# Performance work log

Measured on AMD Instinct MI355X. Metric: run time of the kernel, lower is better.

The kernel has to match this reference:

```python
import jax, jax.numpy as jnp
import numpy as np

N = 50000
E = 800000
D_IN = 128
D_H = 128
D_OUT = 1


def setup_inputs() -> dict:
    key = jax.random.key(0)
    ks = jax.random.split(key, 12)
    x = jax.random.normal(ks[0], (N, D_IN), dtype=jnp.float32)
    edge_index = jax.random.randint(ks[1], (2, E), 0, N, dtype=jnp.int64)
    def glorot(k, shape):
        lim = float(np.sqrt(6.0 / (shape[0] + shape[1])))
        return jax.random.uniform(k, shape, jnp.float32, -lim, lim)
    return {
        "x": x,
        "edge_index": edge_index,
        "W1": glorot(ks[2], (D_IN, D_H)),  "b1": jnp.zeros((D_H,), jnp.float32),
        "W2": glorot(ks[3], (D_H, D_H)),   "b2": jnp.zeros((D_H,), jnp.float32),
        "W3": glorot(ks[4], (D_H, D_H)),   "b3": jnp.zeros((D_H,), jnp.float32),
        "Wfc": glorot(ks[5], (D_H, D_OUT)), "bfc": jnp.zeros((D_OUT,), jnp.float32),
    }


def _gcn_norm(edge_index, num_nodes):
    # Add self-loops (PyG GCNConv default) and compute symmetric normalization
    loops = jnp.arange(num_nodes, dtype=edge_index.dtype)
    src = jnp.concatenate([edge_index[0], loops])
    dst = jnp.concatenate([edge_index[1], loops])
    ones = jnp.ones(src.shape[0], dtype=jnp.float32)
    deg = jax.ops.segment_sum(ones, dst, num_segments=num_nodes)
    dinv = jnp.where(deg > 0, jax.lax.rsqrt(deg), 0.0)
    norm = dinv[src] * dinv[dst]  # [E + N]
    return src, dst, norm


def _gcn_layer(x, W, b, src, dst, norm, num_nodes):
    xw = x @ W                              # [N, out] dense transform first
    msg = xw[src] * norm[:, None]           # gather + scale
    agg = jax.ops.segment_sum(msg, dst, num_segments=num_nodes)  # scatter-add
    return agg + b


def reference(x, edge_index, W1, b1, W2, b2, W3, b3, Wfc, bfc):
    num_nodes = x.shape[0]
    src, dst, norm = _gcn_norm(edge_index, num_nodes)
    h = jax.nn.relu(_gcn_layer(x, W1, b1, src, dst, norm, num_nodes))
    h = jax.nn.relu(_gcn_layer(h, W2, b2, src, dst, norm, num_nodes))
    h = jax.nn.relu(_gcn_layer(h, W3, b3, src, dst, norm, num_nodes))
    return h @ Wfc + bfc  # [N, 1]
```

## Files before the change

kernel.cpp:

```cpp
#include <hip/hip_runtime.h>

#define D 128
#define SCAN_ELEMS 4096

typedef __attribute__((ext_vector_type(8))) short short8;
typedef __attribute__((ext_vector_type(4))) float f32x4;


__global__ void count_kernel(const int* __restrict__ dst, int* __restrict__ deg,
                             int* __restrict__ rank, int e) {
    int i = blockIdx.x * blockDim.x + threadIdx.x;
    if (i < e) rank[i] = atomicAdd(&deg[dst[i]], 1);
}

__global__ __launch_bounds__(256) void scanA_kernel(const int* __restrict__ deg,
                                                    int* __restrict__ blkSums, int n) {
    __shared__ int waveSums[4];
    int t = threadIdx.x;
    int base = blockIdx.x * SCAN_ELEMS + t * 16;
    int s = 0;
    if (base + 16 <= n) {
        const int4* p = reinterpret_cast<const int4*>(deg + base);
        #pragma unroll
        for (int k = 0; k < 4; ++k) {
            int4 v = p[k];
            s += v.x + v.y + v.z + v.w;
        }
    } else {
        for (int k = 0; k < 16; ++k) {
            int i = base + k;
            if (i < n) s += deg[i];
        }
    }
    #pragma unroll
    for (int off = 32; off > 0; off >>= 1) s += __shfl_down(s, off);
    int lane = t & 63, w = t >> 6;
    if (lane == 0) waveSums[w] = s;
    __syncthreads();
    if (t == 0) blkSums[blockIdx.x] = waveSums[0] + waveSums[1] + waveSums[2] + waveSums[3];
}

__global__ __launch_bounds__(256) void scanC_kernel(const int* __restrict__ deg,
                                                    const int* __restrict__ blkSums,
                                                    int* __restrict__ offsets,
                                                    float* __restrict__ dinv, int n, int nblk) {
    __shared__ int waveSums[4];
    __shared__ int blkBase;
    int t = threadIdx.x;
    int lane = t & 63, w = t >> 6;

    if (t < 64) {
        int s = (t < nblk && t < blockIdx.x) ? blkSums[t] : 0;
        #pragma unroll
        for (int off = 32; off > 0; off >>= 1) s += __shfl_down(s, off);
        if (t == 0) blkBase = s;
    }

    int base = blockIdx.x * SCAN_ELEMS + t * 16;
    int v[16];
    int s = 0;
    #pragma unroll
    for (int k = 0; k < 16; ++k) {
        int i = base + k;
        int d = (i < n) ? deg[i] : 0;
        v[k] = d;
        s += d;
    }
    int incl = s;
    #pragma unroll
    for (int off = 1; off < 64; off <<= 1) {
        int u = __shfl_up(incl, off);
        if (lane >= off) incl += u;
    }
    if (lane == 63) waveSums[w] = incl;
    __syncthreads();
    int waveOff = 0;
    for (int i = 0; i < 4; ++i) if (i < w) waveOff += waveSums[i];
    int off0 = blkBase + waveOff + incl - s;

    #pragma unroll
    for (int k = 0; k < 16; ++k) {
        int i = base + k;
        if (i < n) {
            offsets[i] = off0;
            dinv[i] = rsqrtf((float)(v[k] + 1));
            off0 += v[k];
        }
    }
}

__global__ void fill_kernel(const int* __restrict__ src, const int* __restrict__ dst,
                            const int* __restrict__ offsets, const int* __restrict__ rank,
                            int* __restrict__ csr_src, int e) {
    int i = blockIdx.x * blockDim.x + threadIdx.x;
    if (i < e) {
        csr_src[offsets[dst[i]] + rank[i]] = src[i];
    }
}

__device__ inline void f2bf(float f, short& hi, short& lo) {
    union { float f; unsigned u; } a; a.f = f;
    unsigned r = a.u + 0x7fffu + ((a.u >> 16) & 1u);
    hi = (short)(r >> 16);
    union { unsigned u; float f; } h; h.u = ((unsigned)(unsigned short)hi) << 16;
    union { float f; unsigned u; } b; b.f = f - h.f;
    unsigned r2 = b.u + 0x7fffu + ((b.u >> 16) & 1u);
    lo = (short)(r2 >> 16);
}

__device__ inline unsigned enc24(float f) {
    union { float f; unsigned u; } a; a.f = f;
    unsigned r = a.u + 0x7fu + ((a.u >> 8) & 1u);
    return r >> 8;
}

__global__ __launch_bounds__(256) void wsplit_kernel(const float* __restrict__ W1,
                                                     const float* __restrict__ W2,
                                                     const float* __restrict__ W3,
                                                     short* __restrict__ Bsw) {
    int tid = blockIdx.x * 256 + threadIdx.x;
    int layer = tid >> 14;
    int rem = tid & 16383;
    int k = rem >> 7, c = rem & 127;
    const float* Wg = (layer == 0) ? W1 : ((layer == 1) ? W2 : W3);
    float v = Wg[k * 128 + c];
    short hi, lo; f2bf(v, hi, lo);
    int ktile = k >> 5, kk = k & 31, q = kk >> 3, j = kk & 7;
    int ct = c >> 4, mm = c & 15, lane = q * 16 + mm;
    int idx = layer * 32768 + ((ktile * 8 + ct) * 64 + lane) * 8 + j;
    Bsw[idx] = hi;
    Bsw[idx + 16384] = lo;
}

__global__ __launch_bounds__(256) void gemm_kernel(const float* __restrict__ A,
                                                   const short* __restrict__ Bsw,
                                                   const float* __restrict__ dinv,
                                                   unsigned short* __restrict__ xh,
                                                   unsigned char* __restrict__ xl, int n) {
    __shared__ float tile[4][16][132];

    int t = threadIdx.x;
    int w = t >> 6;
    int lane = t & 63;
    int quad = lane >> 4;
    int m = lane & 15;

    int rowBase = blockIdx.x * 64 + w * 16;
    int arow = rowBase + m;
    bool valid = arow < n;
    const float* ap = A + (size_t)(valid ? arow : 0) * D + quad * 8;

    f32x4 acc[8];
    #pragma unroll
    for (int ct = 0; ct < 8; ++ct) acc[ct] = (f32x4){0.f, 0.f, 0.f, 0.f};

    #pragma unroll
    for (int kt = 0; kt < 4; ++kt) {
        short8 a_hi, a_lo;
        {
            float4 f0 = *reinterpret_cast<const float4*>(ap + kt * 32);
            float4 f1 = *reinterpret_cast<const float4*>(ap + kt * 32 + 4);
            float fv[8] = {f0.x, f0.y, f0.z, f0.w, f1.x, f1.y, f1.z, f1.w};
            #pragma unroll
            for (int j = 0; j < 8; ++j) {
                short h, l; f2bf(valid ? fv[j] : 0.f, h, l);
                a_hi[j] = h; a_lo[j] = l;
            }
        }
        const short* bp = Bsw + (kt * 8 * 64 + lane) * 8;
        #pragma unroll
        for (int ct = 0; ct < 8; ++ct) {
            short8 b_hi = *reinterpret_cast<const short8*>(bp + ct * 512);
            short8 b_lo = *reinterpret_cast<const short8*>(bp + 16384 + ct * 512);
            acc[ct] = __builtin_amdgcn_mfma_f32_16x16x32_bf16(a_hi, b_hi, acc[ct], 0, 0, 0);
            acc[ct] = __builtin_amdgcn_mfma_f32_16x16x32_bf16(a_hi, b_lo, acc[ct], 0, 0, 0);
            acc[ct] = __builtin_amdgcn_mfma_f32_16x16x32_bf16(a_lo, b_hi, acc[ct], 0, 0, 0);
        }
    }

    #pragma unroll
    for (int r = 0; r < 4; ++r) {
        int orow = rowBase + quad * 4 + r;
        float s = (orow < n) ? dinv[orow] : 0.f;
        #pragma unroll
        for (int ct = 0; ct < 8; ++ct)
            tile[w][quad * 4 + r][m + ct * 16] = acc[ct][r] * s;
    }
    __syncthreads();

    int r = lane >> 2;
    int c0 = (lane & 3) << 5;
    int gr = rowBase + r;
    if (gr < n) {
        unsigned hu[16], lu[8];
        #pragma unroll
        for (int g = 0; g < 8; ++g) {
            float4 f = *reinterpret_cast<const float4*>(&tile[w][r][c0 + g * 4]);
            unsigned e0 = enc24(f.x), e1 = enc24(f.y), e2 = enc24(f.z), e3 = enc24(f.w);
            hu[g * 2]     = (e0 >> 8) | ((e1 >> 8) << 16);
            hu[g * 2 + 1] = (e2 >> 8) | ((e3 >> 8) << 16);
            lu[g] = (e0 & 0xffu) | ((e1 & 0xffu) << 8) | ((e2 & 0xffu) << 16) | ((e3 & 0xffu) << 24);
        }
        uint4* hp = reinterpret_cast<uint4*>(xh + (size_t)gr * 128 + c0);
        uint4* lp = reinterpret_cast<uint4*>(xl + (size_t)gr * 128 + c0);
        hp[0] = *reinterpret_cast<uint4*>(&hu[0]);
        hp[1] = *reinterpret_cast<uint4*>(&hu[4]);
        hp[2] = *reinterpret_cast<uint4*>(&hu[8]);
        hp[3] = *reinterpret_cast<uint4*>(&hu[12]);
        lp[0] = *reinterpret_cast<uint4*>(&lu[0]);
        lp[1] = *reinterpret_cast<uint4*>(&lu[4]);
    }
}


__device__ inline void g24(const unsigned short* __restrict__ xh,
                           const unsigned char* __restrict__ xl,
                           int row, int c, float4& a) {
    uint2 h2 = *reinterpret_cast<const uint2*>(xh + (size_t)row * 128 + c);
    unsigned lb = *reinterpret_cast<const unsigned*>(xl + (size_t)row * 128 + c);
    union { unsigned u; float f; } v0, v1, v2, v3;
    v0.u = ((h2.x & 0xffffu) << 16) | ((lb & 0xffu) << 8);
    v1.u = (h2.x & 0xffff0000u)     | (((lb >> 8) & 0xffu) << 8);
    v2.u = ((h2.y & 0xffffu) << 16) | (((lb >> 16) & 0xffu) << 8);
    v3.u = (h2.y & 0xffff0000u)     | ((lb >> 24) << 8);
    a.x += v0.f; a.y += v1.f; a.z += v2.f; a.w += v3.f;
}

__global__ __launch_bounds__(256) void agg_kernel(const unsigned short* __restrict__ xh,
                                                  const unsigned char* __restrict__ xl,
                                                  const int* __restrict__ csr_src,
                                                  const int* __restrict__ offsets,
                                                  const int* __restrict__ deg,
                                                  const float* __restrict__ dinv,
                                                  const float* __restrict__ bias,
                                                  float* __restrict__ outp,
                                                  const float* __restrict__ fcw,
                                                  const float* __restrict__ fcb,
                                                  float* __restrict__ fcout,
                                                  int n) {
    int wave = (blockIdx.x * blockDim.x + threadIdx.x) >> 6;
    int lane = threadIdx.x & 63;
    if (wave >= n) return;
    int node = wave;
    int half = lane >> 5;
    int l32  = lane & 31;
    int col  = l32 << 2;

    int base = offsets[node];
    int cnt  = deg[node];

    float di = dinv[node];
    float4 vs = make_float4(0.f, 0.f, 0.f, 0.f);
    g24(xh, xl, node, col, vs);
    float4 b = *reinterpret_cast<const float4*>(bias + col);

    float4 acc0 = make_float4(0.f, 0.f, 0.f, 0.f);
    float4 acc1 = make_float4(0.f, 0.f, 0.f, 0.f);
    float4 acc2 = make_float4(0.f, 0.f, 0.f, 0.f);
    float4 acc3 = make_float4(0.f, 0.f, 0.f, 0.f);

    if (cnt <= 64) {
        int idx = (lane < cnt) ? csr_src[base + lane] : 0;
        int j = 0;
        for (; j + 8 <= cnt; j += 8) {
            int s0 = __shfl(idx, j     + half);
            int s1 = __shfl(idx, j + 2 + half);
            int s2 = __shfl(idx, j + 4 + half);
            int s3 = __shfl(idx, j + 6 + half);
            g24(xh, xl, s0, col, acc0);
            g24(xh, xl, s1, col, acc1);
            g24(xh, xl, s2, col, acc2);
            g24(xh, xl, s3, col, acc3);
        }
        for (; j + 2 <= cnt; j += 2) {
            int s0 = __shfl(idx, j + half);
            g24(xh, xl, s0, col, acc0);
        }
        if (j < cnt) {
            int s0 = __shfl(idx, j);
            if (half == 0) g24(xh, xl, s0, col, acc1);
        }
    } else {
        int j = 0;
        for (; j + 2 <= cnt; j += 2) {
            int s = csr_src[base + j + half];
            g24(xh, xl, s, col, acc0);
        }
        if (j < cnt && half == 0) {
            int s = csr_src[base + j];
            g24(xh, xl, s, col, acc1);
        }
    }

    acc0.x += acc1.x + acc2.x + acc3.x;
    acc0.y += acc1.y + acc2.y + acc3.y;
    acc0.z += acc1.z + acc2.z + acc3.z;
    acc0.w += acc1.w + acc2.w + acc3.w;
    acc0.x += __shfl_down(acc0.x, 32);
    acc0.y += __shfl_down(acc0.y, 32);
    acc0.z += __shfl_down(acc0.z, 32);
    acc0.w += __shfl_down(acc0.w, 32);

    float4 r;
    r.x = fmaxf(di * (acc0.x + vs.x) + b.x, 0.f);
    r.y = fmaxf(di * (acc0.y + vs.y) + b.y, 0.f);
    r.z = fmaxf(di * (acc0.z + vs.z) + b.z, 0.f);
    r.w = fmaxf(di * (acc0.w + vs.w) + b.w, 0.f);

    if (fcw == nullptr) {
        if (half == 0)
            *reinterpret_cast<float4*>(outp + (size_t)node * D + col) = r;
    } else {
        float4 wv = *reinterpret_cast<const float4*>(fcw + col);
        float s = (half == 0) ? (r.x * wv.x + r.y * wv.y + r.z * wv.z + r.w * wv.w) : 0.f;
        #pragma unroll
        for (int off = 32; off > 0; off >>= 1) s += __shfl_down(s, off);
        if (lane == 0) fcout[node] = s + fcb[0];
    }
}


extern "C" void kernel_launch(void* const* d_in, const int* in_sizes, int n_in,
                              void* d_out, int out_size, void* d_ws, size_t ws_size,
                              hipStream_t stream) {
    const float* x   = (const float*)d_in[0];
    const int*   ei  = (const int*)d_in[1];
    const float* W1  = (const float*)d_in[2];
    const float* b1  = (const float*)d_in[3];
    const float* W2  = (const float*)d_in[4];
    const float* b2  = (const float*)d_in[5];
    const float* W3  = (const float*)d_in[6];
    const float* b3  = (const float*)d_in[7];
    const float* Wfc = (const float*)d_in[8];
    const float* bfc = (const float*)d_in[9];
    float* outp = (float*)d_out;

    const int n = in_sizes[0] / D;
    const int e = in_sizes[1] / 2;
    const int* src = ei;
    const int* dst = ei + e;

    char* ws = (char*)d_ws;
    size_t off = 0;
    auto alloc = [&](size_t bytes) {
        void* p = ws + off;
        off += (bytes + 255) & ~(size_t)255;
        return p;
    };
    int*            deg     = (int*)alloc((size_t)n * 4);
    size_t          zero_bytes = off;
    int*            offsets = (int*)alloc((size_t)n * 4);
    float*          dinv    = (float*)alloc((size_t)n * 4);
    int*            blkSums = (int*)alloc(64 * 4);
    short*          Bsw     = (short*)alloc((size_t)3 * 32768 * 2);
    int*            rank    = (int*)alloc((size_t)e * 4);
    int*            csr_src = (int*)alloc((size_t)e * 4);
    unsigned short* xhbuf   = (unsigned short*)alloc((size_t)n * 128 * 2);
    unsigned char*  xlbuf   = (unsigned char*)alloc((size_t)n * 128);
    float*          buf1    = (float*)alloc((size_t)n * D * 4);

    int eb256 = (e + 255) / 256;
    int scan_blocks = (n + SCAN_ELEMS - 1) / SCAN_ELEMS;

    hipMemsetAsync(ws, 0, zero_bytes, stream);
    count_kernel <<<eb256, 256, 0, stream>>>(dst, deg, rank, e);
    scanA_kernel <<<scan_blocks, 256, 0, stream>>>(deg, blkSums, n);
    scanC_kernel <<<scan_blocks, 256, 0, stream>>>(deg, blkSums, offsets, dinv, n, scan_blocks);
    fill_kernel  <<<eb256, 256, 0, stream>>>(src, dst, offsets, rank, csr_src, e);
    wsplit_kernel<<<192, 256, 0, stream>>>(W1, W2, W3, Bsw);

    int gemm_blocks = (n + 63) / 64;
    int agg_blocks  = (n + 3) / 4;

    gemm_kernel<<<gemm_blocks, 256, 0, stream>>>(x, Bsw, dinv, xhbuf, xlbuf, n);
    agg_kernel <<<agg_blocks, 256, 0, stream>>>(xhbuf, xlbuf, csr_src, offsets, deg, dinv, b1, buf1,
                                                nullptr, nullptr, nullptr, n);
    gemm_kernel<<<gemm_blocks, 256, 0, stream>>>(buf1, Bsw + 32768, dinv, xhbuf, xlbuf, n);
    agg_kernel <<<agg_blocks, 256, 0, stream>>>(xhbuf, xlbuf, csr_src, offsets, deg, dinv, b2, buf1,
                                                nullptr, nullptr, nullptr, n);
    gemm_kernel<<<gemm_blocks, 256, 0, stream>>>(buf1, Bsw + 65536, dinv, xhbuf, xlbuf, n);
    agg_kernel <<<agg_blocks, 256, 0, stream>>>(xhbuf, xlbuf, csr_src, offsets, deg, dinv, b3, nullptr,
                                                Wfc, bfc, outp, n);
}
```

Measured before the change: 334.8 us.

## Slice feature layout by column and fuse setup kernels into combined launches

Stores the transformed features in eight column-slice planes (slice-major, 16 columns per row) so the aggregation can run one block per node-group per slice, aiming to keep each slice's gather working set cache-resident. The GEMM now writes the encoded outputs directly with scattered 2-byte and 1-byte stores instead of staging through shared memory. The count and weight-split kernels are merged into one launch, and the CSR fill is merged with the first GEMM, to cut launch count. The final layer keeps a whole-node kernel adapted to the new layout. Risks include uncoalesced narrow stores in the GEMM, re-reading CSR indices eight times, and low lane utilization in small-degree aggregation.

New measurement: 615.9 us. 1.84x slower.

```diff
diff --git a/kernel.cpp b/kernel.cpp
--- a/kernel.cpp
+++ b/kernel.cpp
@@ -6,11 +6,67 @@
 typedef __attribute__((ext_vector_type(8))) short short8;
 typedef __attribute__((ext_vector_type(4))) float f32x4;
 
-
-__global__ void count_kernel(const int* __restrict__ dst, int* __restrict__ deg,
-                             int* __restrict__ rank, int e) {
-    int i = blockIdx.x * blockDim.x + threadIdx.x;
-    if (i < e) rank[i] = atomicAdd(&deg[dst[i]], 1);
+__device__ inline void f2bf(float f, short& hi, short& lo) {
+    union { float f; unsigned u; } a; a.f = f;
+    unsigned r = a.u + 0x7fffu + ((a.u >> 16) & 1u);
+    hi = (short)(r >> 16);
+    union { unsigned u; float f; } h; h.u = ((unsigned)(unsigned short)hi) << 16;
+    union { float f; unsigned u; } b; b.f = f - h.f;
+    unsigned r2 = b.u + 0x7fffu + ((b.u >> 16) & 1u);
+    lo = (short)(r2 >> 16);
+}
+
+__device__ inline unsigned enc24(float f) {
+    union { float f; unsigned u; } a; a.f = f;
+    unsigned r = a.u + 0x7fu + ((a.u >> 8) & 1u);
+    return r >> 8;
+}
+
+__device__ inline void dec4(const unsigned short* __restrict__ xh,
+                            const unsigned char* __restrict__ xl,
+                            unsigned off, float* a) {
+    uint2 h2 = *reinterpret_cast<const uint2*>(xh + off);
+    unsigned lb = *reinterpret_cast<const unsigned*>(xl + off);
+    union { unsigned u; float f; } v0, v1, v2, v3;
+    v0.u = ((h2.x & 0xffffu) << 16) | ((lb & 0xffu) << 8);
+    v1.u = (h2.x & 0xffff0000u)     | (((lb >> 8) & 0xffu) << 8);
+    v2.u = ((h2.y & 0xffffu) << 16) | (((lb >> 16) & 0xffu) << 8);
+    v3.u = (h2.y & 0xffff0000u)     | ((lb >> 24) << 8);
+    a[0] += v0.f; a[1] += v1.f; a[2] += v2.f; a[3] += v3.f;
+}
+
+
+__device__ void wsplit_body(int tid, const float* __restrict__ W1,
+                            const float* __restrict__ W2, const float* __restrict__ W3,
+                            short* __restrict__ Bsw) {
+    int layer = tid >> 14;
+    int rem = tid & 16383;
+    int k = rem >> 7, c = rem & 127;
+    const float* Wg = (layer == 0) ? W1 : ((layer == 1) ? W2 : W3);
+    float v = Wg[k * 128 + c];
+    short hi, lo; f2bf(v, hi, lo);
+    int ktile = k >> 5, kk = k & 31, q = kk >> 3, j = kk & 7;
+    int ct = c >> 4, mm = c & 15, lane = q * 16 + mm;
+    int idx = layer * 32768 + ((ktile * 8 + ct) * 64 + lane) * 8 + j;
+    Bsw[idx] = hi;
+    Bsw[idx + 16384] = lo;
+}
+
+__global__ __launch_bounds__(256) void count_wsplit_kernel(const int* __restrict__ dst,
+                                                           int* __restrict__ deg,
+                                                           int* __restrict__ rank, int e,
+                                                           int nbCount,
+                                                           const float* __restrict__ W1,
+                                                           const float* __restrict__ W2,
+                                                           const float* __restrict__ W3,
+                                                           short* __restrict__ Bsw) {
+    if ((int)blockIdx.x < nbCount) {
+        int i = blockIdx.x * 256 + threadIdx.x;
+        if (i < e) rank[i] = atomicAdd(&deg[dst[i]], 1);
+    } else {
+        int tid = (blockIdx.x - nbCount) * 256 + threadIdx.x;
+        wsplit_body(tid, W1, W2, W3, Bsw);
+    }
 }
 
 __global__ __launch_bounds__(256) void scanA_kernel(const int* __restrict__ deg,
@@ -50,7 +106,7 @@
     int lane = t & 63, w = t >> 6;
 
     if (t < 64) {
-        int s = (t < nblk && t < blockIdx.x) ? blkSums[t] : 0;
+        int s = (t < nblk && t < (int)blockIdx.x) ? blkSums[t] : 0;
         #pragma unroll
         for (int off = 32; off > 0; off >>= 1) s += __shfl_down(s, off);
         if (t == 0) blkBase = s;
@@ -89,63 +145,17 @@
     }
 }
 
-__global__ void fill_kernel(const int* __restrict__ src, const int* __restrict__ dst,
-                            const int* __restrict__ offsets, const int* __restrict__ rank,
-                            int* __restrict__ csr_src, int e) {
-    int i = blockIdx.x * blockDim.x + threadIdx.x;
-    if (i < e) {
-        csr_src[offsets[dst[i]] + rank[i]] = src[i];
-    }
-}
-
-__device__ inline void f2bf(float f, short& hi, short& lo) {
-    union { float f; unsigned u; } a; a.f = f;
-    unsigned r = a.u + 0x7fffu + ((a.u >> 16) & 1u);
-    hi = (short)(r >> 16);
-    union { unsigned u; float f; } h; h.u = ((unsigned)(unsigned short)hi) << 16;
-    union { float f; unsigned u; } b; b.f = f - h.f;
-    unsigned r2 = b.u + 0x7fffu + ((b.u >> 16) & 1u);
-    lo = (short)(r2 >> 16);
-}
-
-__device__ inline unsigned enc24(float f) {
-    union { float f; unsigned u; } a; a.f = f;
-    unsigned r = a.u + 0x7fu + ((a.u >> 8) & 1u);
-    return r >> 8;
-}
-
-__global__ __launch_bounds__(256) void wsplit_kernel(const float* __restrict__ W1,
-                                                     const float* __restrict__ W2,
-                                                     const float* __restrict__ W3,
-                                                     short* __restrict__ Bsw) {
-    int tid = blockIdx.x * 256 + threadIdx.x;
-    int layer = tid >> 14;
-    int rem = tid & 16383;
-    int k = rem >> 7, c = rem & 127;
-    const float* Wg = (layer == 0) ? W1 : ((layer == 1) ? W2 : W3);
-    float v = Wg[k * 128 + c];
-    short hi, lo; f2bf(v, hi, lo);
-    int ktile = k >> 5, kk = k & 31, q = kk >> 3, j = kk & 7;
-    int ct = c >> 4, mm = c & 15, lane = q * 16 + mm;
-    int idx = layer * 32768 + ((ktile * 8 + ct) * 64 + lane) * 8 + j;
-    Bsw[idx] = hi;
-    Bsw[idx + 16384] = lo;
-}
-
-__global__ __launch_bounds__(256) void gemm_kernel(const float* __restrict__ A,
-                                                   const short* __restrict__ Bsw,
-                                                   const float* __restrict__ dinv,
-                                                   unsigned short* __restrict__ xh,
-                                                   unsigned char* __restrict__ xl, int n) {
-    __shared__ float tile[4][16][132];
-
-    int t = threadIdx.x;
+__device__ void gemm_body(int blk, const float* __restrict__ A,
+                          const short* __restrict__ Bsw,
+                          const float* __restrict__ dinv,
+                          unsigned short* __restrict__ xh,
+                          unsigned char* __restrict__ xl, int n, int t) {
     int w = t >> 6;
     int lane = t & 63;
     int quad = lane >> 4;
     int m = lane & 15;
 
-    int rowBase = blockIdx.x * 64 + w * 16;
+    int rowBase = blk * 64 + w * 16;
     int arow = rowBase + m;
     bool valid = arow < n;
     const float* ap = A + (size_t)(valid ? arow : 0) * D + quad * 8;
@@ -167,7 +177,7 @@
                 a_hi[j] = h; a_lo[j] = l;
             }
         }
-        const short* bp = Bsw + (kt * 8 * 64 + lane) * 8;
+        const short* bp = Bsw + (kt * 512 + lane) * 8;
         #pragma unroll
         for (int ct = 0; ct < 8; ++ct) {
             short8 b_hi = *reinterpret_cast<const short8*>(bp + ct * 512);
@@ -180,84 +190,140 @@
 
     #pragma unroll
     for (int r = 0; r < 4; ++r) {
-        int orow = rowBase + quad * 4 + r;
-        float s = (orow < n) ? dinv[orow] : 0.f;
+        int row = rowBase + quad * 4 + r;
+        if (row < n) {
+            float s = dinv[row];
+            #pragma unroll
+            for (int ct = 0; ct < 8; ++ct) {
+                unsigned e24 = enc24(acc[ct][r] * s);
+                unsigned off = ((unsigned)ct * (unsigned)n + (unsigned)row) * 16u + (unsigned)m;
+                xh[off] = (unsigned short)(e24 >> 8);
+                xl[off] = (unsigned char)(e24 & 0xffu);
+            }
+        }
+    }
+}
+
+__global__ __launch_bounds__(256) void gemm_kernel(const float* __restrict__ A,
+                                                   const short* __restrict__ Bsw,
+                                                   const float* __restrict__ dinv,
+                                                   unsigned short* __restrict__ xh,
+                                                   unsigned char* __restrict__ xl, int n) {
+    gemm_body(blockIdx.x, A, Bsw, dinv, xh, xl, n, threadIdx.x);
+}
+
+__global__ __launch_bounds__(256) void fill_gemm_kernel(const int* __restrict__ src,
+                                                        const int* __restrict__ dst,
+                                                        const int* __restrict__ offsets,
+                                                        const int* __restrict__ rank,
+                                                        int* __restrict__ csr_src, int e,
+                                                        int nbFill,
+                                                        const float* __restrict__ A,
+                                                        const short* __restrict__ Bsw,
+                                                        const float* __restrict__ dinv,
+                                                        unsigned short* __restrict__ xh,
+                                                        unsigned char* __restrict__ xl, int n) {
+    if ((int)blockIdx.x < nbFill) {
+        int i = blockIdx.x * 256 + threadIdx.x;
+        if (i < e) csr_src[offsets[dst[i]] + rank[i]] = src[i];
+    } else {
+        gemm_body(blockIdx.x - nbFill, A, Bsw, dinv, xh, xl, n, threadIdx.x);
+    }
+}
+
+__global__ __launch_bounds__(256) void aggs_kernel(const unsigned short* __restrict__ xh,
+                                                   const unsigned char* __restrict__ xl,
+                                                   const int* __restrict__ csr_src,
+                                                   const int* __restrict__ offsets,
+                                                   const int* __restrict__ deg,
+                                                   const float* __restrict__ dinv,
+                                                   const float* __restrict__ bias,
+                                                   float* __restrict__ outp, int n) {
+    int b = blockIdx.x;
+    int slice = b & 7;
+    int w = threadIdx.x >> 6;
+    int node = (b >> 3) * 4 + w;
+    if (node >= n) return;
+    int lane = threadIdx.x & 63;
+    int e16 = lane & 15;
+    int g = lane >> 4;
+
+    unsigned sbase = (unsigned)slice * (unsigned)n;
+    unsigned g4 = (unsigned)(g << 2);
+
+    int base = offsets[node];
+    int cnt  = deg[node];
+    float di = dinv[node];
+
+    float vs[4] = {};
+    dec4(xh, xl, (sbase + (unsigned)node) * 16u + g4, vs);
+    float4 bb = *reinterpret_cast<const float4*>(bias + slice * 16 + (g << 2));
+
+    float a[4] = {};
+    if (cnt <= 64) {
+        int idx = (lane < cnt) ? csr_src[base + lane] : 0;
+        for (int j = 0; j < cnt; j += 16) {
+            int eI = j + e16;
+            int s0 = __shfl(idx, eI);
+            if (eI < cnt)
+                dec4(xh, xl, (sbase + (unsigned)s0) * 16u + g4, a);
+        }
+    } else {
+        for (int j = 0; j < cnt; j += 16) {
+            int eI = j + e16;
+            if (eI < cnt) {
+                int s0 = csr_src[base + eI];
+                dec4(xh, xl, (sbase + (unsigned)s0) * 16u + g4, a);
+            }
+        }
+    }
+
+    #pragma unroll
+    for (int s = 1; s < 16; s <<= 1) {
         #pragma unroll
-        for (int ct = 0; ct < 8; ++ct)
-            tile[w][quad * 4 + r][m + ct * 16] = acc[ct][r] * s;
-    }
-    __syncthreads();
-
-    int r = lane >> 2;
-    int c0 = (lane & 3) << 5;
-    int gr = rowBase + r;
-    if (gr < n) {
-        unsigned hu[16], lu[8];
-        #pragma unroll
-        for (int g = 0; g < 8; ++g) {
-            float4 f = *reinterpret_cast<const float4*>(&tile[w][r][c0 + g * 4]);
-            unsigned e0 = enc24(f.x), e1 = enc24(f.y), e2 = enc24(f.z), e3 = enc24(f.w);
-            hu[g * 2]     = (e0 >> 8) | ((e1 >> 8) << 16);
-            hu[g * 2 + 1] = (e2 >> 8) | ((e3 >> 8) << 16);
-            lu[g] = (e0 & 0xffu) | ((e1 & 0xffu) << 8) | ((e2 & 0xffu) << 16) | ((e3 & 0xffu) << 24);
-        }
-        uint4* hp = reinterpret_cast<uint4*>(xh + (size_t)gr * 128 + c0);
-        uint4* lp = reinterpret_cast<uint4*>(xl + (size_t)gr * 128 + c0);
-        hp[0] = *reinterpret_cast<uint4*>(&hu[0]);
-        hp[1] = *reinterpret_cast<uint4*>(&hu[4]);
-        hp[2] = *reinterpret_cast<uint4*>(&hu[8]);
-        hp[3] = *reinterpret_cast<uint4*>(&hu[12]);
-        lp[0] = *reinterpret_cast<uint4*>(&lu[0]);
-        lp[1] = *reinterpret_cast<uint4*>(&lu[4]);
-    }
-}
-
-
-__device__ inline void g24(const unsigned short* __restrict__ xh,
-                           const unsigned char* __restrict__ xl,
-                           int row, int c, float4& a) {
-    uint2 h2 = *reinterpret_cast<const uint2*>(xh + (size_t)row * 128 + c);
-    unsigned lb = *reinterpret_cast<const unsigned*>(xl + (size_t)row * 128 + c);
-    union { unsigned u; float f; } v0, v1, v2, v3;
-    v0.u = ((h2.x & 0xffffu) << 16) | ((lb & 0xffu) << 8);
-    v1.u = (h2.x & 0xffff0000u)     | (((lb >> 8) & 0xffu) << 8);
-    v2.u = ((h2.y & 0xffffu) << 16) | (((lb >> 16) & 0xffu) << 8);
-    v3.u = (h2.y & 0xffff0000u)     | ((lb >> 24) << 8);
-    a.x += v0.f; a.y += v1.f; a.z += v2.f; a.w += v3.f;
-}
-
-__global__ __launch_bounds__(256) void agg_kernel(const unsigned short* __restrict__ xh,
-                                                  const unsigned char* __restrict__ xl,
-                                                  const int* __restrict__ csr_src,
-                                                  const int* __restrict__ offsets,
-                                                  const int* __restrict__ deg,
-                                                  const float* __restrict__ dinv,
-                                                  const float* __restrict__ bias,
-                                                  float* __restrict__ outp,
-                                                  const float* __restrict__ fcw,
-                                                  const float* __restrict__ fcb,
-                                                  float* __restrict__ fcout,
-                                                  int n) {
+        for (int k = 0; k < 4; ++k) a[k] += __shfl_down(a[k], s);
+    }
+
+    if (e16 == 0) {
+        float4 r;
+        r.x = fmaxf(di * (a[0] + vs[0]) + bb.x, 0.f);
+        r.y = fmaxf(di * (a[1] + vs[1]) + bb.y, 0.f);
+        r.z = fmaxf(di * (a[2] + vs[2]) + bb.z, 0.f);
+        r.w = fmaxf(di * (a[3] + vs[3]) + bb.w, 0.f);
+        *reinterpret_cast<float4*>(outp + (size_t)node * D + slice * 16 + (g << 2)) = r;
+    }
+}
+
+__global__ __launch_bounds__(256) void aggf_kernel(const unsigned short* __restrict__ xh,
+                                                   const unsigned char* __restrict__ xl,
+                                                   const int* __restrict__ csr_src,
+                                                   const int* __restrict__ offsets,
+                                                   const int* __restrict__ deg,
+                                                   const float* __restrict__ dinv,
+                                                   const float* __restrict__ bias,
+                                                   const float* __restrict__ fcw,
+                                                   const float* __restrict__ fcb,
+                                                   float* __restrict__ fcout, int n) {
     int wave = (blockIdx.x * blockDim.x + threadIdx.x) >> 6;
     int lane = threadIdx.x & 63;
     if (wave >= n) return;
     int node = wave;
     int half = lane >> 5;
     int l32  = lane & 31;
-    int col  = l32 << 2;
+    unsigned srow = (unsigned)(l32 >> 2);
+    unsigned cp   = (unsigned)((l32 & 3) << 2);
+    int colb = (int)(srow * 16 + cp);
+    unsigned sb = srow * (unsigned)n;
 
     int base = offsets[node];
     int cnt  = deg[node];
-
     float di = dinv[node];
-    float4 vs = make_float4(0.f, 0.f, 0.f, 0.f);
-    g24(xh, xl, node, col, vs);
-    float4 b = *reinterpret_cast<const float4*>(bias + col);
-
-    float4 acc0 = make_float4(0.f, 0.f, 0.f, 0.f);
-    float4 acc1 = make_float4(0.f, 0.f, 0.f, 0.f);
-    float4 acc2 = make_float4(0.f, 0.f, 0.f, 0.f);
-    float4 acc3 = make_float4(0.f, 0.f, 0.f, 0.f);
+
+    float vs[4] = {};
+    dec4(xh, xl, (sb + (unsigned)node) * 16u + cp, vs);
+    float4 bb = *reinterpret_cast<const float4*>(bias + colb);
+
+    float a0[4] = {}, a1[4] = {}, a2[4] = {}, a3[4] = {};
 
     if (cnt <= 64) {
         int idx = (lane < cnt) ? csr_src[base + lane] : 0;
@@ -267,56 +333,49 @@
             int s1 = __shfl(idx, j + 2 + half);
             int s2 = __shfl(idx, j + 4 + half);
             int s3 = __shfl(idx, j + 6 + half);
-            g24(xh, xl, s0, col, acc0);
-            g24(xh, xl, s1, col, acc1);
-            g24(xh, xl, s2, col, acc2);
-            g24(xh, xl, s3, col, acc3);
+            dec4(xh, xl, (sb + (unsigned)s0) * 16u + cp, a0);
+            dec4(xh, xl, (sb + (unsigned)s1) * 16u + cp, a1);
+            dec4(xh, xl, (sb + (unsigned)s2) * 16u + cp, a2);
+            dec4(xh, xl, (sb + (unsigned)s3) * 16u + cp, a3);
         }
         for (; j + 2 <= cnt; j += 2) {
             int s0 = __shfl(idx, j + half);
-            g24(xh, xl, s0, col, acc0);
+            dec4(xh, xl, (sb + (unsigned)s0) * 16u + cp, a0);
         }
         if (j < cnt) {
             int s0 = __shfl(idx, j);
-            if (half == 0) g24(xh, xl, s0, col, acc1);
+            if (half == 0) dec4(xh, xl, (sb + (unsigned)s0) * 16u + cp, a1);
         }
     } else {
         int j = 0;
         for (; j + 2 <= cnt; j += 2) {
             int s = csr_src[base + j + half];
-            g24(xh, xl, s, col, acc0);
+            dec4(xh, xl, (sb + (unsigned)s) * 16u + cp, a0);
         }
         if (j < cnt && half == 0) {
             int s = csr_src[base + j];
-            g24(xh, xl, s, col, acc1);
-        }
-    }
-
-    acc0.x += acc1.x + acc2.x + acc3.x;
-    acc0.y += acc1.y + acc2.y + acc3.y;
-    acc0.z += acc1.z + acc2.z + acc3.z;
-    acc0.w += acc1.w + acc2.w + acc3.w;
-    acc0.x += __shfl_down(acc0.x, 32);
-    acc0.y += __shfl_down(acc0.y, 32);
-    acc0.z += __shfl_down(acc0.z, 32);
-    acc0.w += __shfl_down(acc0.w, 32);
-
-    float4 r;
-    r.x = fmaxf(di * (acc0.x + vs.x) + b.x, 0.f);
-    r.y = fmaxf(di * (acc0.y + vs.y) + b.y, 0.f);
-    r.z = fmaxf(di * (acc0.z + vs.z) + b.z, 0.f);
-    r.w = fmaxf(di * (acc0.w + vs.w) + b.w, 0.f);
-
-    if (fcw == nullptr) {
-        if (half == 0)
-            *reinterpret_cast<float4*>(outp + (size_t)node * D + col) = r;
-    } else {
-        float4 wv = *reinterpret_cast<const float4*>(fcw + col);
-        float s = (half == 0) ? (r.x * wv.x + r.y * wv.y + r.z * wv.z + r.w * wv.w) : 0.f;
-        #pragma unroll
-        for (int off = 32; off > 0; off >>= 1) s += __shfl_down(s, off);
-        if (lane == 0) fcout[node] = s + fcb[0];
-    }
+            dec4(xh, xl, (sb + (unsigned)s) * 16u + cp, a1);
+        }
+    }
+
+    #pragma unroll
+    for (int k = 0; k < 4; ++k) {
+        a0[k] += a1[k] + a2[k] + a3[k];
+        a0[k] += __shfl_down(a0[k], 32);
+    }
+
+    float4 wv = *reinterpret_cast<const float4*>(fcw + colb);
+    float s = 0.f;
+    if (half == 0) {
+        float r0 = fmaxf(di * (a0[0] + vs[0]) + bb.x, 0.f);
+        float r1 = fmaxf(di * (a0[1] + vs[1]) + bb.y, 0.f);
+        float r2 = fmaxf(di * (a0[2] + vs[2]) + bb.z, 0.f);
+        float r3 = fmaxf(di * (a0[3] + vs[3]) + bb.w, 0.f);
+        s = r0 * wv.x + r1 * wv.y + r2 * wv.z + r3 * wv.w;
+    }
+    #pragma unroll
+    for (int off = 32; off > 0; off >>= 1) s += __shfl_down(s, off);
+    if (lane == 0) fcout[node] = s + fcb[0];
 }
 
 
@@ -361,24 +420,24 @@
 
     int eb256 = (e + 255) / 256;
     int scan_blocks = (n + SCAN_ELEMS - 1) / SCAN_ELEMS;
+    int gemm_blocks = (n + 63) / 64;
+    int aggs_blocks = ((n + 3) / 4) * 8;
+    int aggf_blocks = (n + 3) / 4;
 
     hipMemsetAsync(ws, 0, zero_bytes, stream);
-    count_kernel <<<eb256, 256, 0, stream>>>(dst, deg, rank, e);
-    scanA_kernel <<<scan_blocks, 256, 0, stream>>>(deg, blkSums, n);
-    scanC_kernel <<<scan_blocks, 256, 0, stream>>>(deg, blkSums, offsets, dinv, n, scan_blocks);
-    fill_kernel  <<<eb256, 256, 0, stream>>>(src, dst, offsets, rank, csr_src, e);
-    wsplit_kernel<<<192, 256, 0, stream>>>(W1, W2, W3, Bsw);
-
-    int gemm_blocks = (n + 63) / 64;
-    int agg_blocks  = (n + 3) / 4;
-
-    gemm_kernel<<<gemm_blocks, 256, 0, stream>>>(x, Bsw, dinv, xhbuf, xlbuf, n);
-    agg_kernel <<<agg_blocks, 256, 0, stream>>>(xhbuf, xlbuf, csr_src, offsets, deg, dinv, b1, buf1,
-                                                nullptr, nullptr, nullptr, n);
+    count_wsplit_kernel<<<eb256 + 192, 256, 0, stream>>>(dst, deg, rank, e, eb256,
+                                                         W1, W2, W3, Bsw);
+    scanA_kernel<<<scan_blocks, 256, 0, stream>>>(deg, blkSums, n);
+    scanC_kernel<<<scan_blocks, 256, 0, stream>>>(deg, blkSums, offsets, dinv, n, scan_blocks);
+    fill_gemm_kernel<<<eb256 + gemm_blocks, 256, 0, stream>>>(src, dst, offsets, rank, csr_src,
+                                                              e, eb256, x, Bsw, dinv,
+                                                              xhbuf, xlbuf, n);
+    aggs_kernel<<<aggs_blocks, 256, 0, stream>>>(xhbuf, xlbuf, csr_src, offsets, deg, dinv,
+                                                 b1, buf1, n);
     gemm_kernel<<<gemm_blocks, 256, 0, stream>>>(buf1, Bsw + 32768, dinv, xhbuf, xlbuf, n);
-    agg_kernel <<<agg_blocks, 256, 0, stream>>>(xhbuf, xlbuf, csr_src, offsets, deg, dinv, b2, buf1,
-                                                nullptr, nullptr, nullptr, n);
+    aggs_kernel<<<aggs_blocks, 256, 0, stream>>>(xhbuf, xlbuf, csr_src, offsets, deg, dinv,
+                                                 b2, buf1, n);
     gemm_kernel<<<gemm_blocks, 256, 0, stream>>>(buf1, Bsw + 65536, dinv, xhbuf, xlbuf, n);
-    agg_kernel <<<agg_blocks, 256, 0, stream>>>(xhbuf, xlbuf, csr_src, offsets, deg, dinv, b3, nullptr,
-                                                Wfc, bfc, outp, n);
-}
+    aggf_kernel<<<aggf_blocks, 256, 0, stream>>>(xhbuf, xlbuf, csr_src, offsets, deg, dinv,
+                                                 b3, Wfc, bfc, outp, n);
+}
```

## Merge count with weight split and fill with first GEMM; shrink CSR indices to u16

Applied to the files above, without the earlier changes.

Fuses the degree-count kernel with the weight-split kernel, and the CSR fill kernel with the first-layer GEMM, using block-index ranges so fewer launches occur and independent work overlaps. Stores rank and CSR source indices as 16-bit values, which halves index traffic in the aggregation gathers but is only valid while node count and degrees stay below 65536. The GEMM epilogue now writes encoded outputs directly instead of staging through shared memory, which drops the LDS tile and barrier but gives narrower, less coalesced stores.

Measured after the change: 336.1 us. About the same (+0.4%).

```diff
diff --git a/kernel.cpp b/kernel.cpp
--- a/kernel.cpp
+++ b/kernel.cpp
@@ -6,11 +6,67 @@
 typedef __attribute__((ext_vector_type(8))) short short8;
 typedef __attribute__((ext_vector_type(4))) float f32x4;
 
-
-__global__ void count_kernel(const int* __restrict__ dst, int* __restrict__ deg,
-                             int* __restrict__ rank, int e) {
-    int i = blockIdx.x * blockDim.x + threadIdx.x;
-    if (i < e) rank[i] = atomicAdd(&deg[dst[i]], 1);
+__device__ inline void f2bf(float f, short& hi, short& lo) {
+    union { float f; unsigned u; } a; a.f = f;
+    unsigned r = a.u + 0x7fffu + ((a.u >> 16) & 1u);
+    hi = (short)(r >> 16);
+    union { unsigned u; float f; } h; h.u = ((unsigned)(unsigned short)hi) << 16;
+    union { float f; unsigned u; } b; b.f = f - h.f;
+    unsigned r2 = b.u + 0x7fffu + ((b.u >> 16) & 1u);
+    lo = (short)(r2 >> 16);
+}
+
+__device__ inline unsigned enc24(float f) {
+    union { float f; unsigned u; } a; a.f = f;
+    unsigned r = a.u + 0x7fu + ((a.u >> 8) & 1u);
+    return r >> 8;
+}
+
+__device__ inline void g24(const unsigned short* __restrict__ xh,
+                           const unsigned char* __restrict__ xl,
+                           int row, int c, float4& a) {
+    uint2 h2 = *reinterpret_cast<const uint2*>(xh + (size_t)row * 128 + c);
+    unsigned lb = *reinterpret_cast<const unsigned*>(xl + (size_t)row * 128 + c);
+    union { unsigned u; float f; } v0, v1, v2, v3;
+    v0.u = (h2.x << 16)          | ((lb << 8) & 0xff00u);
+    v1.u = (h2.x & 0xffff0000u)  | (lb & 0xff00u);
+    v2.u = (h2.y << 16)          | ((lb >> 8) & 0xff00u);
+    v3.u = (h2.y & 0xffff0000u)  | ((lb >> 16) & 0xff00u);
+    a.x += v0.f; a.y += v1.f; a.z += v2.f; a.w += v3.f;
+}
+
+
+__device__ void wsplit_body(int tid, const float* __restrict__ W1,
+                            const float* __restrict__ W2, const float* __restrict__ W3,
+                            short* __restrict__ Bsw) {
+    int layer = tid >> 14;
+    int rem = tid & 16383;
+    int k = rem >> 7, c = rem & 127;
+    const float* Wg = (layer == 0) ? W1 : ((layer == 1) ? W2 : W3);
+    float v = Wg[k * 128 + c];
+    short hi, lo; f2bf(v, hi, lo);
+    int ktile = k >> 5, kk = k & 31, q = kk >> 3, j = kk & 7;
+    int ct = c >> 4, mm = c & 15, lane = q * 16 + mm;
+    int idx = layer * 32768 + ((ktile * 8 + ct) * 64 + lane) * 8 + j;
+    Bsw[idx] = hi;
+    Bsw[idx + 16384] = lo;
+}
+
+__global__ __launch_bounds__(256) void count_wsplit_kernel(const int* __restrict__ dst,
+                                                           int* __restrict__ deg,
+                                                           unsigned short* __restrict__ rank,
+                                                           int e, int nbCount,
+                                                           const float* __restrict__ W1,
+                                                           const float* __restrict__ W2,
+                                                           const float* __restrict__ W3,
+                                                           short* __restrict__ Bsw) {
+    if ((int)blockIdx.x < nbCount) {
+        int i = blockIdx.x * 256 + threadIdx.x;
+        if (i < e) rank[i] = (unsigned short)atomicAdd(&deg[dst[i]], 1);
+    } else {
+        int tid = (blockIdx.x - nbCount) * 256 + threadIdx.x;
+        wsplit_body(tid, W1, W2, W3, Bsw);
+    }
 }
 
 __global__ __launch_bounds__(256) void scanA_kernel(const int* __restrict__ deg,
@@ -50,7 +106,7 @@
     int lane = t & 63, w = t >> 6;
 
     if (t < 64) {
-        int s = (t < nblk && t < blockIdx.x) ? blkSums[t] : 0;
+        int s = (t < nblk && t < (int)blockIdx.x) ? blkSums[t] : 0;
         #pragma unroll
         for (int off = 32; off > 0; off >>= 1) s += __shfl_down(s, off);
         if (t == 0) blkBase = s;
@@ -89,63 +145,17 @@
     }
 }
 
-__global__ void fill_kernel(const int* __restrict__ src, const int* __restrict__ dst,
-                            const int* __restrict__ offsets, const int* __restrict__ rank,
-                            int* __restrict__ csr_src, int e) {
-    int i = blockIdx.x * blockDim.x + threadIdx.x;
-    if (i < e) {
-        csr_src[offsets[dst[i]] + rank[i]] = src[i];
-    }
-}
-
-__device__ inline void f2bf(float f, short& hi, short& lo) {
-    union { float f; unsigned u; } a; a.f = f;
-    unsigned r = a.u + 0x7fffu + ((a.u >> 16) & 1u);
-    hi = (short)(r >> 16);
-    union { unsigned u; float f; } h; h.u = ((unsigned)(unsigned short)hi) << 16;
-    union { float f; unsigned u; } b; b.f = f - h.f;
-    unsigned r2 = b.u + 0x7fffu + ((b.u >> 16) & 1u);
-    lo = (short)(r2 >> 16);
-}
-
-__device__ inline unsigned enc24(float f) {
-    union { float f; unsigned u; } a; a.f = f;
-    unsigned r = a.u + 0x7fu + ((a.u >> 8) & 1u);
-    return r >> 8;
-}
-
-__global__ __launch_bounds__(256) void wsplit_kernel(const float* __restrict__ W1,
-                                                     const float* __restrict__ W2,
-                                                     const float* __restrict__ W3,
-                                                     short* __restrict__ Bsw) {
-    int tid = blockIdx.x * 256 + threadIdx.x;
-    int layer = tid >> 14;
-    int rem = tid & 16383;
-    int k = rem >> 7, c = rem & 127;
-    const float* Wg = (layer == 0) ? W1 : ((layer == 1) ? W2 : W3);
-    float v = Wg[k * 128 + c];
-    short hi, lo; f2bf(v, hi, lo);
-    int ktile = k >> 5, kk = k & 31, q = kk >> 3, j = kk & 7;
-    int ct = c >> 4, mm = c & 15, lane = q * 16 + mm;
-    int idx = layer * 32768 + ((ktile * 8 + ct) * 64 + lane) * 8 + j;
-    Bsw[idx] = hi;
-    Bsw[idx + 16384] = lo;
-}
-
-__global__ __launch_bounds__(256) void gemm_kernel(const float* __restrict__ A,
-                                                   const short* __restrict__ Bsw,
-                                                   const float* __restrict__ dinv,
-                                                   unsigned short* __restrict__ xh,
-                                                   unsigned char* __restrict__ xl, int n) {
-    __shared__ float tile[4][16][132];
-
-    int t = threadIdx.x;
+__device__ void gemm_body(int blk, const float* __restrict__ A,
+                          const short* __restrict__ Bsw,
+                          const float* __restrict__ dinv,
+                          unsigned short* __restrict__ xh,
+                          unsigned char* __restrict__ xl, int n, int t) {
     int w = t >> 6;
     int lane = t & 63;
     int quad = lane >> 4;
     int m = lane & 15;
 
-    int rowBase = blockIdx.x * 64 + w * 16;
+    int rowBase = blk * 64 + w * 16;
     int arow = rowBase + m;
     bool valid = arow < n;
     const float* ap = A + (size_t)(valid ? arow : 0) * D + quad * 8;
@@ -167,7 +177,7 @@
                 a_hi[j] = h; a_lo[j] = l;
             }
         }
-        const short* bp = Bsw + (kt * 8 * 64 + lane) * 8;
+        const short* bp = Bsw + (kt * 512 + lane) * 8;
         #pragma unroll
         for (int ct = 0; ct < 8; ++ct) {
             short8 b_hi = *reinterpret_cast<const short8*>(bp + ct * 512);
@@ -180,55 +190,50 @@
 
     #pragma unroll
     for (int r = 0; r < 4; ++r) {
-        int orow = rowBase + quad * 4 + r;
-        float s = (orow < n) ? dinv[orow] : 0.f;
-        #pragma unroll
-        for (int ct = 0; ct < 8; ++ct)
-            tile[w][quad * 4 + r][m + ct * 16] = acc[ct][r] * s;
-    }
-    __syncthreads();
-
-    int r = lane >> 2;
-    int c0 = (lane & 3) << 5;
-    int gr = rowBase + r;
-    if (gr < n) {
-        unsigned hu[16], lu[8];
-        #pragma unroll
-        for (int g = 0; g < 8; ++g) {
-            float4 f = *reinterpret_cast<const float4*>(&tile[w][r][c0 + g * 4]);
-            unsigned e0 = enc24(f.x), e1 = enc24(f.y), e2 = enc24(f.z), e3 = enc24(f.w);
-            hu[g * 2]     = (e0 >> 8) | ((e1 >> 8) << 16);
-            hu[g * 2 + 1] = (e2 >> 8) | ((e3 >> 8) << 16);
-            lu[g] = (e0 & 0xffu) | ((e1 & 0xffu) << 8) | ((e2 & 0xffu) << 16) | ((e3 & 0xffu) << 24);
-        }
-        uint4* hp = reinterpret_cast<uint4*>(xh + (size_t)gr * 128 + c0);
-        uint4* lp = reinterpret_cast<uint4*>(xl + (size_t)gr * 128 + c0);
-        hp[0] = *reinterpret_cast<uint4*>(&hu[0]);
-        hp[1] = *reinterpret_cast<uint4*>(&hu[4]);
-        hp[2] = *reinterpret_cast<uint4*>(&hu[8]);
-        hp[3] = *reinterpret_cast<uint4*>(&hu[12]);
-        lp[0] = *reinterpret_cast<uint4*>(&lu[0]);
-        lp[1] = *reinterpret_cast<uint4*>(&lu[4]);
-    }
-}
-
-
-__device__ inline void g24(const unsigned short* __restrict__ xh,
-                           const unsigned char* __restrict__ xl,
-                           int row, int c, float4& a) {
-    uint2 h2 = *reinterpret_cast<const uint2*>(xh + (size_t)row * 128 + c);
-    unsigned lb = *reinterpret_cast<const unsigned*>(xl + (size_t)row * 128 + c);
-    union { unsigned u; float f; } v0, v1, v2, v3;
-    v0.u = ((h2.x & 0xffffu) << 16) | ((lb & 0xffu) << 8);
-    v1.u = (h2.x & 0xffff0000u)     | (((lb >> 8) & 0xffu) << 8);
-    v2.u = ((h2.y & 0xffffu) << 16) | (((lb >> 16) & 0xffu) << 8);
-    v3.u = (h2.y & 0xffff0000u)     | ((lb >> 24) << 8);
-    a.x += v0.f; a.y += v1.f; a.z += v2.f; a.w += v3.f;
+        int row = rowBase + quad * 4 + r;
+        if (row < n) {
+            float s = dinv[row];
+            size_t rb = (size_t)row * 128 + m;
+            #pragma unroll
+            for (int ct = 0; ct < 8; ++ct) {
+                unsigned e24 = enc24(acc[ct][r] * s);
+                xh[rb + ct * 16] = (unsigned short)(e24 >> 8);
+                xl[rb + ct * 16] = (unsigned char)(e24 & 0xffu);
+            }
+        }
+    }
+}
+
+__global__ __launch_bounds__(256) void gemm_kernel(const float* __restrict__ A,
+                                                   const short* __restrict__ Bsw,
+                                                   const float* __restrict__ dinv,
+                                                   unsigned short* __restrict__ xh,
+                                                   unsigned char* __restrict__ xl, int n) {
+    gemm_body(blockIdx.x, A, Bsw, dinv, xh, xl, n, threadIdx.x);
+}
+
+__global__ __launch_bounds__(256) void fill_gemm_kernel(const int* __restrict__ src,
+                                                        const int* __restrict__ dst,
+                                                        const int* __restrict__ offsets,
+                                                        const unsigned short* __restrict__ rank,
+                                                        unsigned short* __restrict__ csr_src,
+                                                        int e, int nbFill,
+                                                        const float* __restrict__ A,
+                                                        const short* __restrict__ Bsw,
+                                                        const float* __restrict__ dinv,
+                                                        unsigned short* __restrict__ xh,
+                                                        unsigned char* __restrict__ xl, int n) {
+    if ((int)blockIdx.x < nbFill) {
+        int i = blockIdx.x * 256 + threadIdx.x;
+        if (i < e) csr_src[offsets[dst[i]] + rank[i]] = (unsigned short)src[i];
+    } else {
+        gemm_body(blockIdx.x - nbFill, A, Bsw, dinv, xh, xl, n, threadIdx.x);
+    }
 }
 
 __global__ __launch_bounds__(256) void agg_kernel(const unsigned short* __restrict__ xh,
                                                   const unsigned char* __restrict__ xl,
-                                                  const int* __restrict__ csr_src,
+                                                  const unsigned short* __restrict__ csr_src,
                                                   const int* __restrict__ offsets,
                                                   const int* __restrict__ deg,
                                                   const float* __restrict__ dinv,
@@ -260,7 +265,7 @@
     float4 acc3 = make_float4(0.f, 0.f, 0.f, 0.f);
 
     if (cnt <= 64) {
-        int idx = (lane < cnt) ? csr_src[base + lane] : 0;
+        int idx = (lane < cnt) ? (int)csr_src[base + lane] : 0;
         int j = 0;
         for (; j + 8 <= cnt; j += 8) {
             int s0 = __shfl(idx, j     + half);
@@ -283,11 +288,11 @@
     } else {
         int j = 0;
         for (; j + 2 <= cnt; j += 2) {
-            int s = csr_src[base + j + half];
+            int s = (int)csr_src[base + j + half];
             g24(xh, xl, s, col, acc0);
         }
         if (j < cnt && half == 0) {
-            int s = csr_src[base + j];
+            int s = (int)csr_src[base + j];
             g24(xh, xl, s, col, acc1);
         }
     }
@@ -353,32 +358,31 @@
     float*          dinv    = (float*)alloc((size_t)n * 4);
     int*            blkSums = (int*)alloc(64 * 4);
     short*          Bsw     = (short*)alloc((size_t)3 * 32768 * 2);
-    int*            rank    = (int*)alloc((size_t)e * 4);
-    int*            csr_src = (int*)alloc((size_t)e * 4);
+    unsigned short* rank    = (unsigned short*)alloc((size_t)e * 2);
+    unsigned short* csr_src = (unsigned short*)alloc((size_t)e * 2);
     unsigned short* xhbuf   = (unsigned short*)alloc((size_t)n * 128 * 2);
     unsigned char*  xlbuf   = (unsigned char*)alloc((size_t)n * 128);
     float*          buf1    = (float*)alloc((size_t)n * D * 4);
 
     int eb256 = (e + 255) / 256;
     int scan_blocks = (n + SCAN_ELEMS - 1) / SCAN_ELEMS;
-
-    hipMemsetAsync(ws, 0, zero_bytes, stream);
-    count_kernel <<<eb256, 256, 0, stream>>>(dst, deg, rank, e);
-    scanA_kernel <<<scan_blocks, 256, 0, stream>>>(deg, blkSums, n);
-    scanC_kernel <<<scan_blocks, 256, 0, stream>>>(deg, blkSums, offsets, dinv, n, scan_blocks);
-    fill_kernel  <<<eb256, 256, 0, stream>>>(src, dst, offsets, rank, csr_src, e);
-    wsplit_kernel<<<192, 256, 0, stream>>>(W1, W2, W3, Bsw);
-
     int gemm_blocks = (n + 63) / 64;
     int agg_blocks  = (n + 3) / 4;
 
-    gemm_kernel<<<gemm_blocks, 256, 0, stream>>>(x, Bsw, dinv, xhbuf, xlbuf, n);
-    agg_kernel <<<agg_blocks, 256, 0, stream>>>(xhbuf, xlbuf, csr_src, offsets, deg, dinv, b1, buf1,
-                                                nullptr, nullptr, nullptr, n);
+    hipMemsetAsync(ws, 0, zero_bytes, stream);
+    count_wsplit_kernel<<<eb256 + 192, 256, 0, stream>>>(dst, deg, rank, e, eb256,
+                                                         W1, W2, W3, Bsw);
+    scanA_kernel<<<scan_blocks, 256, 0, stream>>>(deg, blkSums, n);
+    scanC_kernel<<<scan_blocks, 256, 0, stream>>>(deg, blkSums, offsets, dinv, n, scan_blocks);
+    fill_gemm_kernel<<<eb256 + gemm_blocks, 256, 0, stream>>>(src, dst, offsets, rank, csr_src,
+                                                              e, eb256, x, Bsw, dinv,
+                                                              xhbuf, xlbuf, n);
+    agg_kernel<<<agg_blocks, 256, 0, stream>>>(xhbuf, xlbuf, csr_src, offsets, deg, dinv, b1, buf1,
+                                               nullptr, nullptr, nullptr, n);
     gemm_kernel<<<gemm_blocks, 256, 0, stream>>>(buf1, Bsw + 32768, dinv, xhbuf, xlbuf, n);
-    agg_kernel <<<agg_blocks, 256, 0, stream>>>(xhbuf, xlbuf, csr_src, offsets, deg, dinv, b2, buf1,
-                                                nullptr, nullptr, nullptr, n);
+    agg_kernel<<<agg_blocks, 256, 0, stream>>>(xhbuf, xlbuf, csr_src, offsets, deg, dinv, b2, buf1,
+                                               nullptr, nullptr, nullptr, n);
     gemm_kernel<<<gemm_blocks, 256, 0, stream>>>(buf1, Bsw + 65536, dinv, xhbuf, xlbuf, n);
-    agg_kernel <<<agg_blocks, 256, 0, stream>>>(xhbuf, xlbuf, csr_src, offsets, deg, dinv, b3, nullptr,
-                                                Wfc, bfc, outp, n);
-}
+    agg_kernel<<<agg_blocks, 256, 0, stream>>>(xhbuf, xlbuf, csr_src, offsets, deg, dinv, b3, nullptr,
+                                               Wfc, bfc, outp, n);
+}
```
